# Kernel tuning notes

Measured on AMD Instinct MI355X. Metric: run time of the kernel, lower is better.

The kernel has to match this reference:

```python
import jax, jax.numpy as jnp
import numpy as np

B, S, D, L = 2, 1024, 1024, 8
HQ, HK, DH = 16, 4, 64          # query heads, kv heads, head_dim = D // HQ
FF, V = 2816, 32000             # FFN hidden (2/3*4D rounded to 256), vocab
EPS = 1e-5
THETA = 500000.0


def setup_inputs() -> dict:
    key = jax.random.key(0)
    ks = jax.random.split(key, 12)
    s = 0.02
    n = lambda k, sh: jax.random.normal(k, sh, dtype=jnp.float32) * s
    return {
        "tokens": jax.random.randint(ks[0], (B, S), 0, V),
        "start_pos": 0,
        "tok_emb": n(ks[1], (V, D)),
        "wq": n(ks[2], (L, D, HQ * DH)),
        "wk": n(ks[3], (L, D, HK * DH)),
        "wv": n(ks[4], (L, D, HK * DH)),
        "wo": n(ks[5], (L, HQ * DH, D)),
        "w1": n(ks[6], (L, D, FF)),
        "w2": n(ks[7], (L, FF, D)),
        "w3": n(ks[8], (L, D, FF)),
        "attn_norm_w": jnp.ones((L, D), jnp.float32),
        "ffn_norm_w": jnp.ones((L, D), jnp.float32),
        "final_norm_w": jnp.ones((D,), jnp.float32),
        "out_w": n(ks[9], (D, V)),
    }


def _rope_cos_sin(start, seqlen):
    freqs = 1.0 / (THETA ** (jnp.arange(0, DH, 2, dtype=jnp.float32) / DH))  # [DH/2]
    t = jnp.arange(start, start + seqlen, dtype=jnp.float32)
    ang = jnp.outer(t, freqs)  # [S, DH/2]
    return jnp.cos(ang), jnp.sin(ang)


def _apply_rope(x, cos, sin):
    # x: [B,S,H,DH]; pairs (even, odd) rotated by complex freqs_cis, as in apply_rotary_emb
    xr = x.reshape(x.shape[:-1] + (DH // 2, 2))
    a, b = xr[..., 0], xr[..., 1]
    c = cos[None, :, None, :]
    s = sin[None, :, None, :]
    out = jnp.stack([a * c - b * s, a * s + b * c], axis=-1)
    return out.reshape(x.shape)


def _rmsnorm(x, w):
    return x * jax.lax.rsqrt(jnp.mean(x * x, axis=-1, keepdims=True) + EPS) * w


def reference(tokens, start_pos, tok_emb, wq, wk, wv, wo, w1, w2, w3,
              attn_norm_w, ffn_norm_w, final_norm_w, out_w):
    h = tok_emb[tokens]  # [B,S,D]
    cos, sin = _rope_cos_sin(start_pos, S)
    # strictly-upper-triangular -inf causal mask (seqlen > 1 branch)
    idx = jnp.arange(S)
    mask = jnp.where(idx[None, :] > idx[:, None], -jnp.inf, 0.0).astype(h.dtype)

    def block(h, p):
        wq_, wk_, wv_, wo_, w1_, w2_, w3_, anw, fnw = p
        x = _rmsnorm(h, anw)
        q = (x @ wq_).reshape(B, S, HQ, DH)
        k = (x @ wk_).reshape(B, S, HK, DH)
        v = (x @ wv_).reshape(B, S, HK, DH)
        q = _apply_rope(q, cos, sin)
        k = _apply_rope(k, cos, sin)
        # start_pos=0: cache slice [:, :seqlen] == freshly written k/v; GQA repeat_kv
        k = jnp.repeat(k, HQ // HK, axis=2)  # [B,S,HQ,DH]
        v = jnp.repeat(v, HQ // HK, axis=2)
        scores = jnp.einsum('bqhd,bkhd->bhqk', q, k) / (DH ** 0.5) + mask
        attn = jax.nn.softmax(scores.astype(jnp.float32), axis=-1).astype(q.dtype)
        o = jnp.einsum('bhqk,bkhd->bqhd', attn, v).reshape(B, S, HQ * DH)
        h = h + o @ wo_
        x2 = _rmsnorm(h, fnw)
        ff = (jax.nn.silu(x2 @ w1_) * (x2 @ w3_)) @ w2_
        return h + ff, None

    h, _ = jax.lax.scan(block, h, (wq, wk, wv, wo, w1, w2, w3, attn_norm_w, ffn_norm_w))
    return (_rmsnorm(h, final_norm_w) @ out_w).astype(jnp.float32)
```

## Files before the change

kernel.cpp:

```cpp
#include <hip/hip_runtime.h>
#include <hip/hip_bf16.h>

typedef __bf16 bf16;
typedef __bf16 bf16x8 __attribute__((ext_vector_type(8)));
typedef float f32x4 __attribute__((ext_vector_type(4)));

#define B_ 2
#define S_ 1024
#define D_ 1024
#define L_ 8
#define HQ_ 16
#define HK_ 4
#define DH_ 64
#define FF_ 2816
#define V_ 32000

#define LGKM0 { asm volatile("s_waitcnt lgkmcnt(0)" ::: "memory"); __builtin_amdgcn_sched_barrier(0); }

__global__ __launch_bounds__(256) void embed_k(const int* __restrict__ toks,
                                               const float* __restrict__ emb,
                                               float* __restrict__ h) {
  int row = blockIdx.x;
  int tok = toks[row];
  f32x4 v = *(const f32x4*)&emb[(size_t)tok * D_ + threadIdx.x * 4];
  *(f32x4*)&h[(size_t)row * D_ + threadIdx.x * 4] = v;
}

__global__ __launch_bounds__(256) void ropetab_k(float* __restrict__ tab) {
  int i = blockIdx.x * 256 + threadIdx.x;
  if (i >= S_ * 32) return;
  int d = i & 31, s = i >> 5;
  float f = expf(-(2.0f * d / 64.0f) * logf(500000.0f));
  float ang = (float)s * f;
  tab[i * 2]     = cosf(ang);
  tab[i * 2 + 1] = sinf(ang);
}

__global__ __launch_bounds__(256) void rmsnorm_k(const float* __restrict__ x,
                                                 const float* __restrict__ w,
                                                 bf16* __restrict__ out) {
  int row = blockIdx.x;
  const float* xr = x + (size_t)row * D_;
  int base = threadIdx.x * 4;
  f32x4 v = *(const f32x4*)&xr[base];
  float ss = v[0]*v[0] + v[1]*v[1] + v[2]*v[2] + v[3]*v[3];
  for (int m = 1; m < 64; m <<= 1) ss += __shfl_xor(ss, m, 64);
  __shared__ float partial[4];
  if ((threadIdx.x & 63) == 0) partial[threadIdx.x >> 6] = ss;
  __syncthreads();
  float tot = partial[0] + partial[1] + partial[2] + partial[3];
  float rr = rsqrtf(tot * (1.0f / D_) + 1e-5f);
  f32x4 wv = *(const f32x4*)&w[base];
  bf16* o = out + (size_t)row * D_ + base;
  o[0] = (bf16)(v[0] * rr * wv[0]);
  o[1] = (bf16)(v[1] * rr * wv[1]);
  o[2] = (bf16)(v[2] * rr * wv[2]);
  o[3] = (bf16)(v[3] * rr * wv[3]);
}

__global__ __launch_bounds__(256) void transpose_cvt(const float* __restrict__ src,
                                                     bf16* __restrict__ dst,
                                                     int K, int N,
                                                     long long srcStride, long long dstStride,
                                                     int rowMul, int rowAdd) {
  __shared__ float tile[32][33];
  int bx = blockIdx.x, by = blockIdx.y, z = blockIdx.z;
  src += (size_t)z * srcStride;
  dst += (size_t)z * dstStride;
  int tx = threadIdx.x & 31, ty = threadIdx.x >> 5;
#pragma unroll
  for (int i = 0; i < 4; ++i) {
    int r = ty + i * 8;
    tile[r][tx] = src[(size_t)(by * 32 + r) * N + bx * 32 + tx];
  }
  __syncthreads();
#pragma unroll
  for (int i = 0; i < 4; ++i) {
    int r = ty + i * 8;
    dst[(size_t)((bx * 32 + r) * rowMul + rowAdd) * K + by * 32 + tx] = (bf16)tile[tx][r];
  }
}

template <int EPI, int BM>
__global__ __launch_bounds__(256) void gemm_bt(const bf16* __restrict__ A,
                                               const bf16* __restrict__ BT,
                                               void* __restrict__ Cout,
                                               const float* __restrict__ R,
                                               int M, int N, int K) {
  constexpr int MR = BM / 32;
  __shared__ bf16 As[BM * 64];
  __shared__ bf16 Bs[128 * 64];
  const int t = threadIdx.x;
  const int w = t >> 6, l = t & 63;
  const int l15 = l & 15, l4 = l >> 4;
  const int bm = blockIdx.x * BM, bn = blockIdx.y * 128;
  const int wr = w >> 1, wc = w & 1;

  const int srow = t >> 3, scol = (t & 7) * 8;
  const bf16* ag = &A[(size_t)(bm + srow) * K + scol];
  const bf16* bg = &BT[(size_t)(bn + srow) * K + scol];
  const int ldsbase = (t & 192) * 8;

  f32x4 acc[MR][4] = {};

  for (int k0 = 0; k0 < K; k0 += 64) {
#pragma unroll
    for (int i = 0; i < BM / 32; ++i)
      __builtin_amdgcn_global_load_lds(
          (const __attribute__((address_space(1))) void*)(ag + (size_t)(i * 32) * K + k0),
          (__attribute__((address_space(3))) void*)&As[i * 2048 + ldsbase], 16, 0, 0);
#pragma unroll
    for (int i = 0; i < 4; ++i)
      __builtin_amdgcn_global_load_lds(
          (const __attribute__((address_space(1))) void*)(bg + (size_t)(i * 32) * K + k0),
          (__attribute__((address_space(3))) void*)&Bs[i * 2048 + ldsbase], 16, 0, 0);
    __syncthreads();
#pragma unroll
    for (int kc = 0; kc < 2; ++kc) {
      bf16x8 af[MR], bfr[4];
#pragma unroll
      for (int m = 0; m < MR; ++m)
        af[m] = *(const bf16x8*)&As[(wr * (BM / 2) + m * 16 + l15) * 64 + kc * 32 + l4 * 8];
#pragma unroll
      for (int n = 0; n < 4; ++n)
        bfr[n] = *(const bf16x8*)&Bs[(wc * 64 + n * 16 + l15) * 64 + kc * 32 + l4 * 8];
#pragma unroll
      for (int m = 0; m < MR; ++m)
#pragma unroll
        for (int n = 0; n < 4; ++n)
          acc[m][n] = __builtin_amdgcn_mfma_f32_16x16x32_bf16(af[m], bfr[n], acc[m][n], 0, 0, 0);
    }
    __syncthreads();
  }

#pragma unroll
  for (int m = 0; m < MR; ++m)
#pragma unroll
    for (int n = 0; n < 4; ++n)
#pragma unroll
      for (int r = 0; r < 4; ++r) {
        int row = bm + wr * (BM / 2) + m * 16 + l4 * 4 + r;
        int col = bn + wc * 64 + n * 16 + l15;
        size_t ix = (size_t)row * N + col;
        float v = acc[m][n][r];
        if (EPI == 0)      ((float*)Cout)[ix] = v;
        else if (EPI == 1) ((float*)Cout)[ix] = v + R[ix];
        else               ((bf16*)Cout)[ix] = (bf16)v;
      }
}

template <int EPI>
__global__ __launch_bounds__(512, 2) void gemm256_bt(const bf16* __restrict__ A,
                                                     const bf16* __restrict__ BT,
                                                     void* __restrict__ Cout,
                                                     const float* __restrict__ R,
                                                     int N, int K) {
  extern __shared__ char smem[];
  const int t = threadIdx.x;
  const int wid = t >> 6, l = t & 63;
  const int l15 = l & 15, l4 = l >> 4;
  const int wr = wid >> 2, wc = wid & 3;
  const int rsw = (l4 ^ ((l15 >> 1) & 3)) * 16;
  const int csw = ((t & 3) ^ ((t >> 3) & 3)) * 8;

  int nwg = gridDim.x;
  int q = nwg >> 3, r = nwg & 7;
  int xcd = blockIdx.x & 7, jj = blockIdx.x >> 3;
  int L = (xcd < r ? xcd * (q + 1) : r * (q + 1) + (xcd - r) * q) + jj;
  const int bm = (L & 7) * 256, bn = (L >> 3) * 256;

  const int NT = K >> 6;

  auto stage = [&](const bf16* __restrict__ G, int rowbase, int cbase, int buf, int kc, int kt) {
#pragma unroll
    for (int i = 0; i < 2; ++i) {
      int j = i * 512 + t;
      const bf16* src = G + (size_t)(rowbase + (j >> 2)) * K + kt * 64 + kc * 32 + csw;
      __builtin_amdgcn_global_load_lds(
          (const __attribute__((address_space(1))) void*)src,
          (__attribute__((address_space(3))) void*)(smem + cbase + buf * 32768 + kc * 16384 +
                                                    i * 8192 + wid * 1024),
          16, 0, 0);
    }
  };
  auto ldA = [&](int buf, int kc, int m) -> bf16x8 {
    return *(const bf16x8*)(smem + buf * 32768 + kc * 16384 +
                            (wr * 128 + m * 16 + l15) * 64 + rsw);
  };
  auto ldB = [&](int buf, int kc, int n) -> bf16x8 {
    return *(const bf16x8*)(smem + 65536 + buf * 32768 + kc * 16384 +
                            (wc * 64 + n * 16 + l15) * 64 + rsw);
  };

  f32x4 acc[8][4] = {};
  bf16x8 af[4], bq[4];

  auto rd03 = [&](int buf, int kc) {
#pragma unroll
    for (int m = 0; m < 4; ++m) af[m] = ldA(buf, kc, m);
#pragma unroll
    for (int n = 0; n < 4; ++n) bq[n] = ldB(buf, kc, n);
  };
  auto rd47 = [&](int buf, int kc) {
#pragma unroll
    for (int m = 0; m < 4; ++m) af[m] = ldA(buf, kc, 4 + m);
  };
  auto mf_lo = [&]() {
    __builtin_amdgcn_s_setprio(1);
#pragma unroll
    for (int m = 0; m < 4; ++m)
#pragma unroll
      for (int n = 0; n < 4; ++n)
        acc[m][n] = __builtin_amdgcn_mfma_f32_16x16x32_bf16(af[m], bq[n], acc[m][n], 0, 0, 0);
    __builtin_amdgcn_s_setprio(0);
    __builtin_amdgcn_sched_barrier(0);
  };
  auto mf_hi = [&]() {
    __builtin_amdgcn_s_setprio(1);
#pragma unroll
    for (int m = 0; m < 4; ++m)
#pragma unroll
      for (int n = 0; n < 4; ++n)
        acc[4 + m][n] = __builtin_amdgcn_mfma_f32_16x16x32_bf16(af[m], bq[n], acc[4 + m][n], 0, 0, 0);
    __builtin_amdgcn_s_setprio(0);
    __builtin_amdgcn_sched_barrier(0);
  };
#define GBAR { __builtin_amdgcn_sched_barrier(0); __builtin_amdgcn_s_barrier(); }
#define VMW(n) { asm volatile("s_waitcnt vmcnt(" #n ")" ::: "memory"); __builtin_amdgcn_sched_barrier(0); }

  stage(A, bm, 0, 0, 0, 0);  stage(BT, bn, 65536, 0, 0, 0);
  stage(A, bm, 0, 0, 1, 0);  stage(BT, bn, 65536, 0, 1, 0);
  stage(A, bm, 0, 1, 0, 1);  stage(BT, bn, 65536, 1, 0, 1);
  VMW(8);
  __builtin_amdgcn_s_barrier();

  for (int kt = 0; kt < NT - 2; ++kt) {
    const int buf = kt & 1, nbuf = buf ^ 1;
    rd03(buf, 0);
    stage(A, bm, 0, nbuf, 1, kt + 1);
    GBAR; mf_lo(); GBAR;
    rd47(buf, 0);
    stage(BT, bn, 65536, nbuf, 1, kt + 1);
    GBAR; mf_hi(); VMW(8); __builtin_amdgcn_s_barrier();
    rd03(buf, 1);
    stage(A, bm, 0, buf, 0, kt + 2);
    stage(BT, bn, 65536, buf, 0, kt + 2);
    GBAR; mf_lo(); GBAR;
    rd47(buf, 1);
    GBAR; mf_hi(); VMW(8); __builtin_amdgcn_s_barrier();
  }
  {
    const int kt = NT - 2;
    const int buf = kt & 1, nbuf = buf ^ 1;
    rd03(buf, 0);
    stage(A, bm, 0, nbuf, 1, kt + 1);
    GBAR; mf_lo(); GBAR;
    rd47(buf, 0);
    stage(BT, bn, 65536, nbuf, 1, kt + 1);
    GBAR; mf_hi(); VMW(8); __builtin_amdgcn_s_barrier();
    rd03(buf, 1);
    GBAR; mf_lo(); GBAR;
    rd47(buf, 1);
    GBAR; mf_hi(); VMW(4); __builtin_amdgcn_s_barrier();
  }
  {
    const int buf = (NT - 1) & 1;
    rd03(buf, 0);
    GBAR; mf_lo(); GBAR;
    rd47(buf, 0);
    GBAR; mf_hi(); VMW(0); __builtin_amdgcn_s_barrier();
    rd03(buf, 1);
    GBAR; mf_lo(); GBAR;
    rd47(buf, 1);
    GBAR; mf_hi(); __builtin_amdgcn_s_barrier();
  }
#undef GBAR
#undef VMW

#pragma unroll
  for (int m = 0; m < 8; ++m)
#pragma unroll
    for (int n = 0; n < 4; ++n)
#pragma unroll
      for (int rr = 0; rr < 4; ++rr) {
        int row = bm + wr * 128 + m * 16 + l4 * 4 + rr;
        int col = bn + wc * 64 + n * 16 + l15;
        size_t ix = (size_t)row * N + col;
        float v = acc[m][n][rr];
        if (EPI == 0)      ((float*)Cout)[ix] = v;
        else if (EPI == 1) ((float*)Cout)[ix] = v + R[ix];
        else               ((bf16*)Cout)[ix] = (bf16)v;
      }
}

template <int EPI>
__global__ __launch_bounds__(512, 4) void gemm8_bt(const bf16* __restrict__ A,
                                                   const bf16* __restrict__ BT,
                                                   void* __restrict__ Cout,
                                                   const float* __restrict__ R,
                                                   int N, int K) {
  extern __shared__ char smem[];
  const int t = threadIdx.x;
  const int wid = t >> 6, l = t & 63;
  const int l15 = l & 15, l4 = l >> 4;
  const int wr = wid >> 1, wc = wid & 1;
  const int rsw = (l4 ^ ((l15 >> 1) & 3)) * 16;
  const int csw = ((t & 3) ^ ((t >> 3) & 3)) * 8;

  int nwg = gridDim.x;
  int q = nwg >> 3;
  int xcd = blockIdx.x & 7, jj = blockIdx.x >> 3;
  int L = xcd * q + jj;
  const int bm = (L & 15) * 128, bn = (L >> 4) * 128;

  const int NT = K >> 6;

  auto stage = [&](const bf16* __restrict__ G, int rowbase, int obase, int buf, int kc, int kt) {
    const bf16* src = G + (size_t)(rowbase + (t >> 2)) * K + kt * 64 + kc * 32 + csw;
    __builtin_amdgcn_global_load_lds(
        (const __attribute__((address_space(1))) void*)src,
        (__attribute__((address_space(3))) void*)(smem + obase + buf * 16384 + kc * 8192 +
                                                  wid * 1024),
        16, 0, 0);
  };
  auto ldA = [&](int buf, int kc, int m) -> bf16x8 {
    return *(const bf16x8*)(smem + buf * 16384 + kc * 8192 +
                            (wr * 32 + m * 16 + l15) * 64 + rsw);
  };
  auto ldB = [&](int buf, int kc, int n) -> bf16x8 {
    return *(const bf16x8*)(smem + 32768 + buf * 16384 + kc * 8192 +
                            (wc * 64 + n * 16 + l15) * 64 + rsw);
  };

  f32x4 acc[2][4] = {};
  bf16x8 af[2], bq[4];

  auto rdph = [&](int buf, int kc) {
#pragma unroll
    for (int m = 0; m < 2; ++m) af[m] = ldA(buf, kc, m);
#pragma unroll
    for (int n = 0; n < 4; ++n) bq[n] = ldB(buf, kc, n);
  };
  auto mf = [&]() {
    __builtin_amdgcn_s_setprio(1);
#pragma unroll
    for (int m = 0; m < 2; ++m)
#pragma unroll
      for (int n = 0; n < 4; ++n)
        acc[m][n] = __builtin_amdgcn_mfma_f32_16x16x32_bf16(af[m], bq[n], acc[m][n], 0, 0, 0);
    __builtin_amdgcn_s_setprio(0);
    __builtin_amdgcn_sched_barrier(0);
  };
#define SCB __builtin_amdgcn_sched_barrier(0)
#define VMW4 { asm volatile("s_waitcnt vmcnt(4)" ::: "memory"); SCB; }
#define VMW2 { asm volatile("s_waitcnt vmcnt(2)" ::: "memory"); SCB; }
#define VMW0 { asm volatile("s_waitcnt vmcnt(0)" ::: "memory"); SCB; }
#define SBAR { __builtin_amdgcn_s_barrier(); SCB; }

  stage(A, bm, 0, 0, 0, 0);  stage(BT, bn, 32768, 0, 0, 0);
  stage(A, bm, 0, 0, 1, 0);  stage(BT, bn, 32768, 0, 1, 0);
  stage(A, bm, 0, 1, 0, 1);  stage(BT, bn, 32768, 1, 0, 1);
  VMW4; __builtin_amdgcn_s_barrier();

  for (int kt = 0; kt < NT - 2; ++kt) {
    const int buf = kt & 1, nbuf = buf ^ 1;
    rdph(buf, 0);
    stage(A, bm, 0, nbuf, 1, kt + 1);
    stage(BT, bn, 32768, nbuf, 1, kt + 1);
    SCB; mf(); VMW4; SBAR;
    rdph(buf, 1);
    stage(A, bm, 0, buf, 0, kt + 2);
    stage(BT, bn, 32768, buf, 0, kt + 2);
    SCB; mf(); VMW4; SBAR;
  }
  {
    const int buf = (NT - 2) & 1, nbuf = buf ^ 1;
    rdph(buf, 0);
    stage(A, bm, 0, nbuf, 1, NT - 1);
    stage(BT, bn, 32768, nbuf, 1, NT - 1);
    SCB; mf(); VMW4; SBAR;
    rdph(buf, 1);
    SCB; mf(); VMW2; SBAR;
  }
  {
    const int buf = (NT - 1) & 1;
    rdph(buf, 0);
    SCB; mf(); VMW0; SBAR;
    rdph(buf, 1);
    SCB; mf();
  }
#undef SCB
#undef VMW4
#undef VMW2
#undef VMW0
#undef SBAR

  if (EPI == 3) {
    bf16* G = (bf16*)Cout;
    const int Nc = N >> 1;
#pragma unroll
    for (int m = 0; m < 2; ++m)
#pragma unroll
      for (int n = 0; n < 4; ++n)
#pragma unroll
        for (int rr = 0; rr < 4; ++rr) {
          float v = acc[m][n][rr];
          float part = __shfl_xor(v, 1, 64);
          if (!(l15 & 1)) {
            float a = v, c = part;
            float s = a / (1.0f + __expf(-a));
            int row = bm + wr * 32 + m * 16 + l4 * 4 + rr;
            int col = (bn >> 1) + wc * 32 + n * 8 + (l15 >> 1);
            G[(size_t)row * Nc + col] = (bf16)(s * c);
          }
        }
  } else {
#pragma unroll
    for (int m = 0; m < 2; ++m)
#pragma unroll
      for (int n = 0; n < 4; ++n)
#pragma unroll
        for (int rr = 0; rr < 4; ++rr) {
          int row = bm + wr * 32 + m * 16 + l4 * 4 + rr;
          int col = bn + wc * 64 + n * 16 + l15;
          size_t ix = (size_t)row * N + col;
          float v = acc[m][n][rr];
          if (EPI == 0)      ((float*)Cout)[ix] = v;
          else               ((bf16*)Cout)[ix] = (bf16)v;
        }
  }
}

__global__ __launch_bounds__(256) void qkvpost_k(const bf16* __restrict__ qkv,
                                                 const float* __restrict__ tab,
                                                 bf16* __restrict__ q_r,
                                                 bf16* __restrict__ k_r,
                                                 bf16* __restrict__ vT) {
  int bid = blockIdx.x, t = threadIdx.x;
  if (bid < 1024) {
    int i = bid * 256 + t;
    int g = i & 7, hh = (i >> 3) & 15, s = (i >> 7) & 1023, b = i >> 17;
    bf16x8 v = *(const bf16x8*)&qkv[(size_t)(b * S_ + s) * 1536 + hh * 64 + g * 8];
    f32x4 tc0 = *(const f32x4*)&tab[(s * 32 + g * 4) * 2];
    f32x4 tc1 = *(const f32x4*)&tab[(s * 32 + g * 4) * 2 + 4];
    bf16x8 o;
#pragma unroll
    for (int j = 0; j < 4; ++j) {
      float a = (float)v[2 * j], bb = (float)v[2 * j + 1];
      float c  = (j < 2 ? tc0 : tc1)[(j & 1) * 2];
      float sn = (j < 2 ? tc0 : tc1)[(j & 1) * 2 + 1];
      o[2 * j]     = (bf16)((a * c - bb * sn) * 0.125f);
      o[2 * j + 1] = (bf16)((a * sn + bb * c) * 0.125f);
    }
    *(bf16x8*)&q_r[((size_t)((b * HQ_ + hh) * S_ + s)) * 64 + g * 8] = o;
  } else if (bid < 1280) {
    int i = (bid - 1024) * 256 + t;
    int g = i & 7, hh = (i >> 3) & 3, s = (i >> 5) & 1023, b = i >> 15;
    bf16x8 v = *(const bf16x8*)&qkv[(size_t)(b * S_ + s) * 1536 + 1024 + hh * 64 + g * 8];
    f32x4 tc0 = *(const f32x4*)&tab[(s * 32 + g * 4) * 2];
    f32x4 tc1 = *(const f32x4*)&tab[(s * 32 + g * 4) * 2 + 4];
    bf16x8 o;
#pragma unroll
    for (int j = 0; j < 4; ++j) {
      float a = (float)v[2 * j], bb = (float)v[2 * j + 1];
      float c  = (j < 2 ? tc0 : tc1)[(j & 1) * 2];
      float sn = (j < 2 ? tc0 : tc1)[(j & 1) * 2 + 1];
      o[2 * j]     = (bf16)(a * c - bb * sn);
      o[2 * j + 1] = (bf16)(a * sn + bb * c);
    }
    *(bf16x8*)&k_r[((size_t)((b * HK_ + hh) * S_ + s)) * 64 + g * 8] = o;
  } else {
    __shared__ bf16 vt[64][66];
    int vb = bid - 1280;
    int b = vb >> 6, hh = (vb >> 4) & 3, s0 = (vb & 15) * 64;
#pragma unroll
    for (int it = 0; it < 2; ++it) {
      int idx = it * 256 + t;
      int s = idx >> 3, g = idx & 7;
      bf16x8 v = *(const bf16x8*)&qkv[(size_t)(b * S_ + s0 + s) * 1536 + 1280 + hh * 64 + g * 8];
      *(bf16x8*)&vt[s][g * 8] = v;
    }
    __syncthreads();
#pragma unroll
    for (int it = 0; it < 2; ++it) {
      int idx = it * 256 + t;
      int dh = idx >> 3, sg = idx & 7;
      bf16x8 o;
#pragma unroll
      for (int j = 0; j < 8; ++j) o[j] = vt[sg * 8 + j][dh];
      *(bf16x8*)&vT[((size_t)((b * HK_ + hh) * 64 + dh)) * S_ + s0 + sg * 8] = o;
    }
  }
}

__global__ __launch_bounds__(256) void attn_k(const bf16* __restrict__ q_r,
                                              const bf16* __restrict__ k_r,
                                              const bf16* __restrict__ vT,
                                              bf16* __restrict__ o) {
  __shared__ bf16 k_lds[64 * 64];
  __shared__ bf16 v_lds[64 * 64];
  __shared__ bf16 p_lds[4][16 * 72];
  int t = threadIdx.x, w = t >> 6, l = t & 63, l15 = l & 15, l4 = l >> 4;
  int bx = blockIdx.x;
  int qt = bx & 15;
  if (bx >= 256) qt = 15 - qt;
  int head = (bx >> 4) & 15, b = bx >> 8;
  int kvh = head >> 2;
  const bf16* qh = q_r + ((size_t)(b * HQ_ + head)) * S_ * 64;
  const bf16* kh = k_r + ((size_t)(b * HK_ + kvh)) * S_ * 64;
  const bf16* vh = vT + ((size_t)(b * HK_ + kvh)) * 64 * S_;
  int q0 = qt * 64 + w * 16;

  bf16x8 aq[2];
  aq[0] = *(const bf16x8*)&qh[(size_t)(q0 + l15) * 64 + l4 * 8];
  aq[1] = *(const bf16x8*)&qh[(size_t)(q0 + l15) * 64 + 32 + l4 * 8];

  f32x4 acc_o[4] = {};
  float m_run[4], l_run[4];
#pragma unroll
  for (int r = 0; r < 4; ++r) { m_run[r] = -1e30f; l_run[r] = 0.f; }

  bf16x8 gk[2], gv[2];
#pragma unroll
  for (int i = 0; i < 2; ++i) {
    int c = i * 256 + t;
    gk[i] = *(const bf16x8*)&kh[c * 8];
    gv[i] = *(const bf16x8*)&vh[(size_t)(c >> 3) * S_ + (c & 7) * 8];
  }

  for (int kt = 0; kt <= qt; ++kt) {
#pragma unroll
    for (int i = 0; i < 2; ++i) {
      int c = i * 256 + t;
      *(bf16x8*)&k_lds[c * 8] = gk[i];
      *(bf16x8*)&v_lds[(c >> 3) * 64 + (c & 7) * 8] = gv[i];
    }
    __syncthreads();

    bf16x8 gkn[2], gvn[2];
    if (kt < qt) {
      const bf16* srck = kh + (kt + 1) * 4096;
#pragma unroll
      for (int i = 0; i < 2; ++i) {
        int c = i * 256 + t;
        gkn[i] = *(const bf16x8*)&srck[c * 8];
        gvn[i] = *(const bf16x8*)&vh[(size_t)(c >> 3) * S_ + (kt + 1) * 64 + (c & 7) * 8];
      }
    }

    f32x4 sc[4];
#pragma unroll
    for (int nt = 0; nt < 4; ++nt) {
      f32x4 a = {};
#pragma unroll
      for (int kc = 0; kc < 2; ++kc) {
        bf16x8 bk = *(const bf16x8*)&k_lds[(nt * 16 + l15) * 64 + kc * 32 + l4 * 8];
        a = __builtin_amdgcn_mfma_f32_16x16x32_bf16(aq[kc], bk, a, 0, 0, 0);
      }
      sc[nt] = a;
    }

    bool diag = (kt == qt);
#pragma unroll
    for (int r = 0; r < 4; ++r) {
      float pmax = -1e30f;
#pragma unroll
      for (int nt = 0; nt < 4; ++nt) {
        float s = sc[nt][r];
        if (diag) {
          int kj = nt * 16 + l15;
          int qi = w * 16 + l4 * 4 + r;
          if (kj > qi) s = -1e30f;
        }
        sc[nt][r] = s;
        pmax = fmaxf(pmax, s);
      }
      if (!__all(pmax <= m_run[r] + 8.0f)) {
        float mx = pmax;
        mx = fmaxf(mx, __shfl_xor(mx, 1, 64));
        mx = fmaxf(mx, __shfl_xor(mx, 2, 64));
        mx = fmaxf(mx, __shfl_xor(mx, 4, 64));
        mx = fmaxf(mx, __shfl_xor(mx, 8, 64));
        float mn = fmaxf(m_run[r], mx);
        float scale = __expf(m_run[r] - mn);
        m_run[r] = mn;
        l_run[r] *= scale;
#pragma unroll
        for (int nt = 0; nt < 4; ++nt) acc_o[nt][r] *= scale;
      }
      float rs = 0.f;
#pragma unroll
      for (int nt = 0; nt < 4; ++nt) {
        float p = __expf(sc[nt][r] - m_run[r]);
        sc[nt][r] = p;
        rs += p;
      }
      rs += __shfl_xor(rs, 1, 64);
      rs += __shfl_xor(rs, 2, 64);
      rs += __shfl_xor(rs, 4, 64);
      rs += __shfl_xor(rs, 8, 64);
      l_run[r] += rs;
    }

#pragma unroll
    for (int nt = 0; nt < 4; ++nt)
#pragma unroll
      for (int r = 0; r < 4; ++r)
        p_lds[w][(l4 * 4 + r) * 72 + nt * 16 + l15] = (bf16)sc[nt][r];
    LGKM0;

#pragma unroll
    for (int kc = 0; kc < 2; ++kc) {
      bf16x8 pf = *(const bf16x8*)&p_lds[w][l15 * 72 + kc * 32 + l4 * 8];
#pragma unroll
      for (int nt = 0; nt < 4; ++nt) {
        bf16x8 vf = *(const bf16x8*)&v_lds[(nt * 16 + l15) * 64 + kc * 32 + l4 * 8];
        acc_o[nt] = __builtin_amdgcn_mfma_f32_16x16x32_bf16(pf, vf, acc_o[nt], 0, 0, 0);
      }
    }
    __syncthreads();

#pragma unroll
    for (int i = 0; i < 2; ++i) { gk[i] = gkn[i]; gv[i] = gvn[i]; }
  }

#pragma unroll
  for (int nt = 0; nt < 4; ++nt)
#pragma unroll
    for (int r = 0; r < 4; ++r) {
      float ov = acc_o[nt][r] / l_run[r];
      int s = qt * 64 + w * 16 + l4 * 4 + r;
      o[((size_t)(b * S_ + s)) * D_ + head * 64 + nt * 16 + l15] = (bf16)ov;
    }
}

extern "C" void kernel_launch(void* const* d_in, const int* in_sizes, int n_in,
                              void* d_out, int out_size, void* d_ws, size_t ws_size,
                              hipStream_t stream) {
  const int* tokens  = (const int*)d_in[0];
  const float* tok_emb = (const float*)d_in[2];
  const float* wq = (const float*)d_in[3];
  const float* wk = (const float*)d_in[4];
  const float* wv = (const float*)d_in[5];
  const float* wo = (const float*)d_in[6];
  const float* w1 = (const float*)d_in[7];
  const float* w2 = (const float*)d_in[8];
  const float* w3 = (const float*)d_in[9];
  const float* anw = (const float*)d_in[10];
  const float* fnw = (const float*)d_in[11];
  const float* finw = (const float*)d_in[12];
  const float* outw = (const float*)d_in[13];

  (void)hipFuncSetAttribute((const void*)gemm256_bt<0>,
                            hipFuncAttributeMaxDynamicSharedMemorySize, 131072);
  (void)hipFuncSetAttribute((const void*)gemm8_bt<2>,
                            hipFuncAttributeMaxDynamicSharedMemorySize, 65536);
  (void)hipFuncSetAttribute((const void*)gemm8_bt<3>,
                            hipFuncAttributeMaxDynamicSharedMemorySize, 65536);

  auto al = [](size_t x) { return (x + 255) & ~(size_t)255; };
  const size_t WTB   = 11272192ull * 2;
  const size_t OUTWTB = (size_t)V_ * D_ * 2;
  const size_t HB   = (size_t)B_ * S_ * D_ * 4;
  const size_t XBB  = (size_t)B_ * S_ * D_ * 2;
  const size_t QKVB = (size_t)B_ * S_ * 1536 * 2;
  const size_t QRB  = (size_t)B_ * HQ_ * S_ * 64 * 2;
  const size_t KRB  = (size_t)B_ * HK_ * S_ * 64 * 2;
  const size_t OB   = (size_t)B_ * S_ * D_ * 2;
  const size_t GATEB = (size_t)B_ * S_ * 2816 * 2;
  const size_t TABB = (size_t)S_ * 32 * 2 * 4;

  size_t fixed = al(OUTWTB) + al(HB) + al(XBB) + al(QKVB) + al(QRB) + al(KRB) + al(KRB) +
                 al(OB) + al(GATEB) + al(TABB);
  bool allup = ws_size >= fixed + 8 * al(WTB) + 4096;
  int nslots = allup ? 8 : 1;

  char* p = (char*)d_ws;
  bf16* wT    = (bf16*)p; p += (size_t)nslots * al(WTB);
  bf16* outwT = (bf16*)p; p += al(OUTWTB);
  float* h    = (float*)p; p += al(HB);
  bf16* xb    = (bf16*)p; p += al(XBB);
  bf16* qkv   = (bf16*)p; p += al(QKVB);
  bf16* q_r   = (bf16*)p; p += al(QRB);
  bf16* k_r   = (bf16*)p; p += al(KRB);
  bf16* vTb   = (bf16*)p; p += al(KRB);
  bf16* ob    = (bf16*)p; p += al(OB);
  bf16* gate  = (bf16*)p; p += al(GATEB);
  float* tab  = (float*)p; p += al(TABB);

  const size_t WTS = al(WTB) / 2;
  const size_t OFF_QKV = 0;
  const size_t OFF_WK  = 1024ull * 1024;
  const size_t OFF_WV  = 1280ull * 1024;
  const size_t OFF_WO  = 1572864ull;
  const size_t OFF_W13 = 2621440ull;
  const size_t OFF_W2  = 8388608ull;

  auto tr = [&](const float* src, size_t srcStride, bf16* dst, size_t dstStride,
                int Kd, int Nd, int layers, int rowMul, int rowAdd) {
    transpose_cvt<<<dim3(Nd / 32, Kd / 32, layers), 256, 0, stream>>>(
        src, dst, Kd, Nd, (long long)srcStride, (long long)dstStride, rowMul, rowAdd);
  };

  ropetab_k<<<128, 256, 0, stream>>>(tab);
  embed_k<<<B_ * S_, 256, 0, stream>>>(tokens, tok_emb, h);
  tr(outw, 0, outwT, 0, 1024, 32000, 1, 1, 0);

  if (allup) {
    tr(wq, 1024 * 1024, wT + OFF_QKV, WTS, 1024, 1024, 8, 1, 0);
    tr(wk, 1024 * 256,  wT + OFF_WK,  WTS, 1024, 256, 8, 1, 0);
    tr(wv, 1024 * 256,  wT + OFF_WV,  WTS, 1024, 256, 8, 1, 0);
    tr(wo, 1024 * 1024, wT + OFF_WO,  WTS, 1024, 1024, 8, 1, 0);
    tr(w1, 1024 * 2816, wT + OFF_W13, WTS, 1024, 2816, 8, 2, 0);
    tr(w3, 1024 * 2816, wT + OFF_W13, WTS, 1024, 2816, 8, 2, 1);
    tr(w2, 2816 * 1024, wT + OFF_W2,  WTS, 2816, 1024, 8, 1, 0);
  }

  for (int l = 0; l < L_; ++l) {
    bf16* wtl = wT + (allup ? (size_t)l * WTS : 0);
    if (!allup) {
      tr(wq + (size_t)l * 1024 * 1024, 0, wtl + OFF_QKV, 0, 1024, 1024, 1, 1, 0);
      tr(wk + (size_t)l * 1024 * 256,  0, wtl + OFF_WK,  0, 1024, 256, 1, 1, 0);
      tr(wv + (size_t)l * 1024 * 256,  0, wtl + OFF_WV,  0, 1024, 256, 1, 1, 0);
      tr(wo + (size_t)l * 1024 * 1024, 0, wtl + OFF_WO,  0, 1024, 1024, 1, 1, 0);
      tr(w1 + (size_t)l * 1024 * 2816, 0, wtl + OFF_W13, 0, 1024, 2816, 1, 2, 0);
      tr(w3 + (size_t)l * 1024 * 2816, 0, wtl + OFF_W13, 0, 1024, 2816, 1, 2, 1);
      tr(w2 + (size_t)l * 2816 * 1024, 0, wtl + OFF_W2,  0, 2816, 1024, 1, 1, 0);
    }

    rmsnorm_k<<<B_ * S_, 256, 0, stream>>>(h, anw + l * D_, xb);
    gemm8_bt<2><<<192, 512, 65536, stream>>>(xb, wtl + OFF_QKV, qkv, nullptr, 1536, 1024);
    qkvpost_k<<<1408, 256, 0, stream>>>(qkv, tab, q_r, k_r, vTb);
    attn_k<<<B_ * HQ_ * (S_ / 64), 256, 0, stream>>>(q_r, k_r, vTb, ob);
    gemm_bt<1, 64><<<dim3(32, 8), 256, 0, stream>>>(ob, wtl + OFF_WO, h, h, 2048, 1024, 1024);
    rmsnorm_k<<<B_ * S_, 256, 0, stream>>>(h, fnw + l * D_, xb);
    gemm8_bt<3><<<704, 512, 65536, stream>>>(xb, wtl + OFF_W13, gate, nullptr, 5632, 1024);
    gemm_bt<1, 64><<<dim3(32, 8), 256, 0, stream>>>(gate, wtl + OFF_W2, h, h, 2048, 1024, 2816);
  }

  rmsnorm_k<<<B_ * S_, 256, 0, stream>>>(h, finw, xb);
  gemm256_bt<0><<<1000, 512, 131072, stream>>>(xb, outwT, d_out, nullptr, 32000, 1024);
}
```

Baseline: 1.673 ms.

## Split-K the W2 down-projection GEMM and swizzle attention K/V LDS layout

The FFN down-projection GEMM (K=2816) is now launched with a split-K grid of two partitions that write fp32 partial sums to a new workspace buffer. A small reduction kernel then adds both partials into the residual. This doubles the block count from 256 to 512 so more CUs are busy, at the cost of extra partial-buffer traffic and one more launch. Separately, the attention kernel XOR-swizzles the K/V tiles in LDS to reduce bank conflicts on the fragment reads.

```diff
diff --git a/kernel.cpp b/kernel.cpp
--- a/kernel.cpp
+++ b/kernel.cpp
@@ -86,7 +86,9 @@
                                                const bf16* __restrict__ BT,
                                                void* __restrict__ Cout,
                                                const float* __restrict__ R,
-                                               int M, int N, int K) {
+                                               int M, int N, int K,
+                                               int lda, int ldb,
+                                               int zKoff, long long partStride) {
   constexpr int MR = BM / 32;
   __shared__ bf16 As[BM * 64];
   __shared__ bf16 Bs[128 * 64];
@@ -95,10 +97,15 @@
   const int l15 = l & 15, l4 = l >> 4;
   const int bm = blockIdx.x * BM, bn = blockIdx.y * 128;
   const int wr = w >> 1, wc = w & 1;
+  const int z = blockIdx.z;
+
+  const bf16* Az = A + (size_t)z * zKoff;
+  const bf16* Bz = BT + (size_t)z * zKoff;
+  float* Cz = (float*)Cout + (size_t)z * partStride;
 
   const int srow = t >> 3, scol = (t & 7) * 8;
-  const bf16* ag = &A[(size_t)(bm + srow) * K + scol];
-  const bf16* bg = &BT[(size_t)(bn + srow) * K + scol];
+  const bf16* ag = &Az[(size_t)(bm + srow) * lda + scol];
+  const bf16* bg = &Bz[(size_t)(bn + srow) * ldb + scol];
   const int ldsbase = (t & 192) * 8;
 
   f32x4 acc[MR][4] = {};
@@ -107,12 +114,12 @@
 #pragma unroll
     for (int i = 0; i < BM / 32; ++i)
       __builtin_amdgcn_global_load_lds(
-          (const __attribute__((address_space(1))) void*)(ag + (size_t)(i * 32) * K + k0),
+          (const __attribute__((address_space(1))) void*)(ag + (size_t)(i * 32) * lda + k0),
           (__attribute__((address_space(3))) void*)&As[i * 2048 + ldsbase], 16, 0, 0);
 #pragma unroll
     for (int i = 0; i < 4; ++i)
       __builtin_amdgcn_global_load_lds(
-          (const __attribute__((address_space(1))) void*)(bg + (size_t)(i * 32) * K + k0),
+          (const __attribute__((address_space(1))) void*)(bg + (size_t)(i * 32) * ldb + k0),
           (__attribute__((address_space(3))) void*)&Bs[i * 2048 + ldsbase], 16, 0, 0);
     __syncthreads();
 #pragma unroll
@@ -143,10 +150,19 @@
         int col = bn + wc * 64 + n * 16 + l15;
         size_t ix = (size_t)row * N + col;
         float v = acc[m][n][r];
-        if (EPI == 0)      ((float*)Cout)[ix] = v;
-        else if (EPI == 1) ((float*)Cout)[ix] = v + R[ix];
-        else               ((bf16*)Cout)[ix] = (bf16)v;
+        if (EPI == 0)      Cz[ix] = v;
+        else               Cz[ix] = v + R[ix];
       }
+}
+
+__global__ __launch_bounds__(256) void reduce2_k(const float* __restrict__ p,
+                                                 float* __restrict__ h) {
+  size_t i = ((size_t)blockIdx.x * 256 + threadIdx.x) * 4;
+  f32x4 a = *(const f32x4*)&p[i];
+  f32x4 b = *(const f32x4*)&p[i + 2097152];
+  f32x4 r = *(const f32x4*)&h[i];
+  r += a + b;
+  *(f32x4*)&h[i] = r;
 }
 
 template <int EPI>
@@ -528,12 +544,15 @@
     gv[i] = *(const bf16x8*)&vh[(size_t)(c >> 3) * S_ + (c & 7) * 8];
   }
 
+  const int swz = l15 & 7;
+
   for (int kt = 0; kt <= qt; ++kt) {
 #pragma unroll
     for (int i = 0; i < 2; ++i) {
       int c = i * 256 + t;
-      *(bf16x8*)&k_lds[c * 8] = gk[i];
-      *(bf16x8*)&v_lds[(c >> 3) * 64 + (c & 7) * 8] = gv[i];
+      int row = c >> 3, ch = (c & 7) ^ (row & 7);
+      *(bf16x8*)&k_lds[row * 64 + ch * 8] = gk[i];
+      *(bf16x8*)&v_lds[row * 64 + ch * 8] = gv[i];
     }
     __syncthreads();
 
@@ -554,7 +573,7 @@
       f32x4 a = {};
 #pragma unroll
       for (int kc = 0; kc < 2; ++kc) {
-        bf16x8 bk = *(const bf16x8*)&k_lds[(nt * 16 + l15) * 64 + kc * 32 + l4 * 8];
+        bf16x8 bk = *(const bf16x8*)&k_lds[(nt * 16 + l15) * 64 + (((kc * 4 + l4) ^ swz) * 8)];
         a = __builtin_amdgcn_mfma_f32_16x16x32_bf16(aq[kc], bk, a, 0, 0, 0);
       }
       sc[nt] = a;
@@ -614,7 +633,7 @@
       bf16x8 pf = *(const bf16x8*)&p_lds[w][l15 * 72 + kc * 32 + l4 * 8];
 #pragma unroll
       for (int nt = 0; nt < 4; ++nt) {
-        bf16x8 vf = *(const bf16x8*)&v_lds[(nt * 16 + l15) * 64 + kc * 32 + l4 * 8];
+        bf16x8 vf = *(const bf16x8*)&v_lds[(nt * 16 + l15) * 64 + (((kc * 4 + l4) ^ swz) * 8)];
         acc_o[nt] = __builtin_amdgcn_mfma_f32_16x16x32_bf16(pf, vf, acc_o[nt], 0, 0, 0);
       }
     }
@@ -669,9 +688,10 @@
   const size_t OB   = (size_t)B_ * S_ * D_ * 2;
   const size_t GATEB = (size_t)B_ * S_ * 2816 * 2;
   const size_t TABB = (size_t)S_ * 32 * 2 * 4;
+  const size_t PARTB = (size_t)B_ * S_ * D_ * 4 * 2;
 
   size_t fixed = al(OUTWTB) + al(HB) + al(XBB) + al(QKVB) + al(QRB) + al(KRB) + al(KRB) +
-                 al(OB) + al(GATEB) + al(TABB);
+                 al(OB) + al(GATEB) + al(TABB) + al(PARTB);
   bool allup = ws_size >= fixed + 8 * al(WTB) + 4096;
   int nslots = allup ? 8 : 1;
 
@@ -687,6 +707,7 @@
   bf16* ob    = (bf16*)p; p += al(OB);
   bf16* gate  = (bf16*)p; p += al(GATEB);
   float* tab  = (float*)p; p += al(TABB);
+  float* part = (float*)p; p += al(PARTB);
 
   const size_t WTS = al(WTB) / 2;
   const size_t OFF_QKV = 0;
@@ -732,10 +753,14 @@
     gemm8_bt<2><<<192, 512, 65536, stream>>>(xb, wtl + OFF_QKV, qkv, nullptr, 1536, 1024);
     qkvpost_k<<<1408, 256, 0, stream>>>(qkv, tab, q_r, k_r, vTb);
     attn_k<<<B_ * HQ_ * (S_ / 64), 256, 0, stream>>>(q_r, k_r, vTb, ob);
-    gemm_bt<1, 64><<<dim3(32, 8), 256, 0, stream>>>(ob, wtl + OFF_WO, h, h, 2048, 1024, 1024);
+    gemm_bt<1, 64><<<dim3(32, 8, 1), 256, 0, stream>>>(ob, wtl + OFF_WO, h, h,
+                                                       2048, 1024, 1024, 1024, 1024, 0, 0);
     rmsnorm_k<<<B_ * S_, 256, 0, stream>>>(h, fnw + l * D_, xb);
     gemm8_bt<3><<<704, 512, 65536, stream>>>(xb, wtl + OFF_W13, gate, nullptr, 5632, 1024);
-    gemm_bt<1, 64><<<dim3(32, 8), 256, 0, stream>>>(gate, wtl + OFF_W2, h, h, 2048, 1024, 2816);
+    gemm_bt<0, 64><<<dim3(32, 8, 2), 256, 0, stream>>>(gate, wtl + OFF_W2, part, nullptr,
+                                                       2048, 1024, 1408, 2816, 2816,
+                                                       1408, 2097152ll);
+    reduce2_k<<<2048, 256, 0, stream>>>(part, h);
   }
 
   rmsnorm_k<<<B_ * S_, 256, 0, stream>>>(h, finw, xb);
```

Measured after the change: 1.537 ms. -8.1%, faster.
